# Performance work log

Hardware: AMD Instinct MI355X
Metric: run time of the kernel (lower is better)

The kernel has to match this reference:

```python
import jax, jax.numpy as jnp
import numpy as np

NBITS = 4
GROUP = 128
K = 4096   # in_features
N = 4096   # out_features
M = 4096   # flattened batch*seq tokens
EPS = 32 // NBITS  # elements per packed int32 = 8
MASK = (1 << NBITS) - 1  # unpack_mask = 15


def setup_inputs() -> dict:
    key = jax.random.key(0)
    k1, k2, k3, k4, k5 = jax.random.split(key, 5)
    x = jax.random.normal(k1, (M, K), dtype=jnp.float32)
    # raw 4-bit quantized weights, layout [K, N] (i.e. W_q.t() from the torch module)
    nib = jax.random.randint(k2, (K, N), 0, 1 << NBITS, dtype=jnp.int32)
    # pack EPS nibbles per int32 along K, matching pack(): element j gets shift j*NBITS
    nib = nib.reshape(K // EPS, EPS, N)
    shifts = (jnp.arange(EPS, dtype=jnp.int32) * NBITS)[None, :, None]
    parts = nib << shifts  # disjoint bit ranges
    W_q_packed = parts[:, 0]
    for j in range(1, EPS):
        W_q_packed = W_q_packed | parts[:, j]
    W_q_packed = W_q_packed.astype(jnp.int32)  # [K//EPS, N]
    # group-wise scales/zeros: [K//GROUP, N] (scales.view(N,-1).t() layout)
    scales = (jax.random.uniform(k3, (K // GROUP, N), dtype=jnp.float32) + 0.5) * 0.01
    zeros = jax.random.uniform(k4, (K // GROUP, N), dtype=jnp.float32) * MASK
    bias = jax.random.normal(k5, (N,), dtype=jnp.float32) * 0.1
    return {"x": x, "W_q_packed": W_q_packed, "scales": scales, "zeros": zeros, "bias": bias}


def reference(x, W_q_packed, scales, zeros, bias):
    # unpack: w[k, n] = (packed[k//EPS, n] >> ((k % EPS) * NBITS)) & MASK
    shifts = (jnp.arange(EPS, dtype=jnp.int32) * NBITS)[None, :, None]
    w = (W_q_packed[:, None, :] >> shifts) & MASK  # [K//EPS, EPS, N]
    w = w.reshape(K, N).astype(jnp.float32)
    # group-wise asymmetric dequant (W_group_mode == 3): W = (w - z) * s
    s = jnp.repeat(scales, GROUP, axis=0)  # [K, N]
    z = jnp.repeat(zeros, GROUP, axis=0)   # [K, N]
    W = (w - z) * s
    out = x @ W + bias  # [M, N]
    return out
```

## Files before the change

kernel.cpp:

```cpp
#include <hip/hip_runtime.h>
#include <stdint.h>


#define M_DIM 4096
#define N_DIM 4096
#define K_DIM 4096

typedef __attribute__((ext_vector_type(8))) short short8;
typedef __attribute__((ext_vector_type(4))) float f32x4;

__device__ __forceinline__ unsigned short f2bf(float f) {
  uint32_t u = __builtin_bit_cast(uint32_t, f);
  u += 0x7fffu + ((u >> 16) & 1u);
  return (unsigned short)(u >> 16);
}

__global__ __launch_bounds__(256) void prep_kernel(const float* __restrict__ x,
                                                   unsigned short* __restrict__ xb,
                                                   const int* __restrict__ Wq,
                                                   const float* __restrict__ scales,
                                                   const float* __restrict__ zeros,
                                                   unsigned short* __restrict__ wt) {
  __shared__ uint4 Ts[32 * 64];
  const int tid = threadIdx.x;
  if (blockIdx.x < 2048) {
    const int total = (M_DIM * K_DIM) / 8;
    const float4* x4 = (const float4*)x;
    uint4* o8 = (uint4*)xb;
#pragma unroll
    for (int p = 0; p < 4; ++p) {
      int i = (p * 2048 + blockIdx.x) * 256 + tid;
      if (i < total) {
        float4 a = x4[2 * i], b = x4[2 * i + 1];
        uint4 o;
        o.x = (uint32_t)f2bf(a.x) | ((uint32_t)f2bf(a.y) << 16);
        o.y = (uint32_t)f2bf(a.z) | ((uint32_t)f2bf(a.w) << 16);
        o.z = (uint32_t)f2bf(b.x) | ((uint32_t)f2bf(b.y) << 16);
        o.w = (uint32_t)f2bf(b.z) | ((uint32_t)f2bf(b.w) << 16);
        o8[i] = o;
      }
    }
    return;
  }
  const int blk = blockIdx.x - 2048;
  const int n0 = (blk & 127) * 32;
  const int gk0 = (blk >> 7) * 64;

#pragma unroll
  for (int p = 0; p < 8; ++p) {
    int e = p * 256 + tid;
    int n_l = e & 31;
    int gk_l = e >> 5;
    int gk = gk0 + gk_l;
    int n = n0 + n_l;
    int g = gk >> 4;
    uint32_t q = (uint32_t)Wq[gk * N_DIM + n];
    float s = scales[g * N_DIM + n];
    float z = zeros[g * N_DIM + n];
    unsigned short b[8];
#pragma unroll
    for (int j = 0; j < 8; ++j) {
      float f = ((float)((q >> (4 * j)) & 15u) - z) * s;
      b[j] = f2bf(f);
    }
    uint4 cell;
    cell.x = (uint32_t)b[0] | ((uint32_t)b[1] << 16);
    cell.y = (uint32_t)b[2] | ((uint32_t)b[3] << 16);
    cell.z = (uint32_t)b[4] | ((uint32_t)b[5] << 16);
    cell.w = (uint32_t)b[6] | ((uint32_t)b[7] << 16);
    Ts[n_l * 64 + (gk_l ^ (n_l & 7))] = cell;
  }
  __syncthreads();
  uint4* dst = (uint4*)wt;
#pragma unroll
  for (int p = 0; p < 8; ++p) {
    int n_l = p * 4 + (tid >> 6);
    int gk_l = tid & 63;
    uint4 cell = Ts[n_l * 64 + (gk_l ^ (n_l & 7))];
    dst[(size_t)(n0 + n_l) * (K_DIM / 8) + (gk0 + gk_l)] = cell;
  }
}

__global__ __launch_bounds__(256) void gemm_bt_kernel(const unsigned short* __restrict__ A,
                                                      const unsigned short* __restrict__ Bt,
                                                      const float* __restrict__ bias,
                                                      float* __restrict__ C) {
  __shared__ short8 As[1024];
  __shared__ short8 Bs[1024];
  const int tid = threadIdx.x;
  const int lane = tid & 63;
  const int w = tid >> 6;
  const int wm = w >> 1, wn = w & 1;

  const int b = blockIdx.x;
  const int xcd = b & 7;
  const int loc = b >> 3;
  const int nt = xcd * 4 + (loc & 3);
  const int mt = loc >> 2;
  const int m0 = mt * 128;
  const int n0 = nt * 128;

  const int c0 = w * 256 + lane;
  const int row0 = c0 >> 3;
  const int kc0 = (c0 & 7) ^ (row0 & 7);
  const unsigned short* Ablk = A + (size_t)m0 * K_DIM;
  const unsigned short* Bblk = Bt + (size_t)n0 * K_DIM;
  const int voff = row0 * K_DIM + kc0 * 8;

  f32x4 acc[4][4] = {};

  const int fr = lane & 15;
  const int fc = lane >> 4;
  const int a_row8 = (wm * 64 + fr) * 8;
  const int b_row8 = (wn * 64 + fr) * 8;
  const int kx0 = fc ^ (fr & 7);
  const int kx1 = (4 + fc) ^ (fr & 7);

  for (int kk = 0; kk < K_DIM / 64; ++kk) {
    const int k0 = kk * 64;
    __syncthreads();
#pragma unroll
    for (int j = 0; j < 4; ++j) {
      __builtin_amdgcn_global_load_lds(
          (const __attribute__((address_space(1))) void*)(Ablk + voff + j * 8 * K_DIM + k0),
          (__attribute__((address_space(3))) void*)&As[c0 + j * 64], 16, 0, 0);
      __builtin_amdgcn_global_load_lds(
          (const __attribute__((address_space(1))) void*)(Bblk + voff + j * 8 * K_DIM + k0),
          (__attribute__((address_space(3))) void*)&Bs[c0 + j * 64], 16, 0, 0);
    }
    __syncthreads();

    {
      short8 af[4], bv[4];
#pragma unroll
      for (int mi = 0; mi < 4; ++mi) af[mi] = As[a_row8 + mi * 128 + kx0];
#pragma unroll
      for (int ni = 0; ni < 4; ++ni) bv[ni] = Bs[b_row8 + ni * 128 + kx0];
#pragma unroll
      for (int mi = 0; mi < 4; ++mi)
#pragma unroll
        for (int ni = 0; ni < 4; ++ni)
          acc[mi][ni] = __builtin_amdgcn_mfma_f32_16x16x32_bf16(af[mi], bv[ni], acc[mi][ni], 0, 0, 0);
    }
    {
      short8 af[4], bv[4];
#pragma unroll
      for (int mi = 0; mi < 4; ++mi) af[mi] = As[a_row8 + mi * 128 + kx1];
#pragma unroll
      for (int ni = 0; ni < 4; ++ni) bv[ni] = Bs[b_row8 + ni * 128 + kx1];
#pragma unroll
      for (int mi = 0; mi < 4; ++mi)
#pragma unroll
        for (int ni = 0; ni < 4; ++ni)
          acc[mi][ni] = __builtin_amdgcn_mfma_f32_16x16x32_bf16(af[mi], bv[ni], acc[mi][ni], 0, 0, 0);
    }
  }

  const int rr = (lane >> 4) * 4;
#pragma unroll
  for (int ni = 0; ni < 4; ++ni) {
    const int gn = n0 + wn * 64 + ni * 16 + fr;
    const float bvv = bias[gn];
#pragma unroll
    for (int mi = 0; mi < 4; ++mi) {
      const int gm = m0 + wm * 64 + mi * 16 + rr;
#pragma unroll
      for (int r = 0; r < 4; ++r)
        C[(size_t)(gm + r) * N_DIM + gn] = acc[mi][ni][r] + bvv;
    }
  }
}

extern "C" void kernel_launch(void* const* d_in, const int* in_sizes, int n_in,
                              void* d_out, int out_size, void* d_ws, size_t ws_size,
                              hipStream_t stream) {
  const float* x = (const float*)d_in[0];
  const int* wq = (const int*)d_in[1];
  const float* sc = (const float*)d_in[2];
  const float* zr = (const float*)d_in[3];
  const float* bias = (const float*)d_in[4];
  float* out = (float*)d_out;

  unsigned short* xb = (unsigned short*)d_ws;
  unsigned short* wt = (unsigned short*)((char*)d_ws + (size_t)M_DIM * K_DIM * 2);

  prep_kernel<<<dim3(3072), dim3(256), 0, stream>>>(x, xb, wq, sc, zr, wt);
  gemm_bt_kernel<<<dim3(1024), dim3(256), 0, stream>>>(xb, wt, bias, out);
}
```

Before: 304.4 us.

## Use 256x256 tiles with double-buffered LDS and phased MFMA scheduling

```diff
diff --git a/kernel.cpp b/kernel.cpp
--- a/kernel.cpp
+++ b/kernel.cpp
@@ -81,79 +81,123 @@
   }
 }
 
-__global__ __launch_bounds__(256) void gemm_bt_kernel(const unsigned short* __restrict__ A,
-                                                      const unsigned short* __restrict__ Bt,
-                                                      const float* __restrict__ bias,
-                                                      float* __restrict__ C) {
-  __shared__ short8 As[1024];
-  __shared__ short8 Bs[1024];
+
+#define STAGE4(DST, SRC)                                                         \
+  {                                                                              \
+    _Pragma("unroll") for (int j = 0; j < 4; ++j)                                \
+        __builtin_amdgcn_global_load_lds(                                        \
+            (const __attribute__((address_space(1))) void*)((SRC) +              \
+                                                            (size_t)j * 64 * K_DIM), \
+            (__attribute__((address_space(3))) void*)((DST) + tid + j * 512),    \
+            16, 0, 0);                                                           \
+  }
+
+#define LOADA(QM)                                                                \
+  {                                                                              \
+    _Pragma("unroll") for (int mi = 0; mi < 4; ++mi) {                           \
+      af[mi][0] = ASb[a_base + ((QM) * 4 + mi) * 128 + kx0];                     \
+      af[mi][1] = ASb[a_base + ((QM) * 4 + mi) * 128 + kx1];                     \
+    }                                                                            \
+  }
+
+#define LOADB(QN)                                                                \
+  {                                                                              \
+    _Pragma("unroll") for (int ni = 0; ni < 2; ++ni) {                           \
+      bv[ni][0] = BSb[b_base + ((QN) * 2 + ni) * 128 + kx0];                     \
+      bv[ni][1] = BSb[b_base + ((QN) * 2 + ni) * 128 + kx1];                     \
+    }                                                                            \
+  }
+
+#define MFMA16(QM, QN)                                                           \
+  {                                                                              \
+    _Pragma("unroll") for (int mi = 0; mi < 4; ++mi)                             \
+        _Pragma("unroll") for (int ni = 0; ni < 2; ++ni) {                       \
+      acc[(QM) * 4 + mi][(QN) * 2 + ni] = __builtin_amdgcn_mfma_f32_16x16x32_bf16( \
+          af[mi][0], bv[ni][0], acc[(QM) * 4 + mi][(QN) * 2 + ni], 0, 0, 0);     \
+      acc[(QM) * 4 + mi][(QN) * 2 + ni] = __builtin_amdgcn_mfma_f32_16x16x32_bf16( \
+          af[mi][1], bv[ni][1], acc[(QM) * 4 + mi][(QN) * 2 + ni], 0, 0, 0);     \
+    }                                                                            \
+  }
+
+#define PHASE_MFMA(QM, QN)                                                       \
+  {                                                                              \
+    __builtin_amdgcn_s_barrier();                                                \
+    __builtin_amdgcn_s_setprio(1);                                               \
+    MFMA16(QM, QN);                                                              \
+    __builtin_amdgcn_s_setprio(0);                                               \
+    __builtin_amdgcn_s_barrier();                                                \
+  }
+
+__global__ __launch_bounds__(512, 2) void gemm_bt_kernel(
+    const unsigned short* __restrict__ A, const unsigned short* __restrict__ Bt,
+    const float* __restrict__ bias, float* __restrict__ C) {
+  __shared__ short8 As[2 * 2048];
+  __shared__ short8 Bs[2 * 2048];
+
   const int tid = threadIdx.x;
   const int lane = tid & 63;
   const int w = tid >> 6;
-  const int wm = w >> 1, wn = w & 1;
+  const int wm = w >> 2;
+  const int wn = w & 3;
 
   const int b = blockIdx.x;
   const int xcd = b & 7;
   const int loc = b >> 3;
-  const int nt = xcd * 4 + (loc & 3);
-  const int mt = loc >> 2;
-  const int m0 = mt * 128;
-  const int n0 = nt * 128;
-
-  const int c0 = w * 256 + lane;
-  const int row0 = c0 >> 3;
-  const int kc0 = (c0 & 7) ^ (row0 & 7);
-  const unsigned short* Ablk = A + (size_t)m0 * K_DIM;
-  const unsigned short* Bblk = Bt + (size_t)n0 * K_DIM;
-  const int voff = row0 * K_DIM + kc0 * 8;
-
-  f32x4 acc[4][4] = {};
+  const int nt = xcd * 2 + (loc & 1);
+  const int mt = loc >> 1;
+  const int m0 = mt * 256;
+  const int n0 = nt * 256;
+
+  const int srow = tid >> 3;
+  const int skc = (tid & 7) ^ (srow & 7);
+  const unsigned short* Ablk = A + (size_t)m0 * K_DIM + (size_t)srow * K_DIM + skc * 8;
+  const unsigned short* Bblk = Bt + (size_t)n0 * K_DIM + (size_t)srow * K_DIM + skc * 8;
 
   const int fr = lane & 15;
   const int fc = lane >> 4;
-  const int a_row8 = (wm * 64 + fr) * 8;
-  const int b_row8 = (wn * 64 + fr) * 8;
-  const int kx0 = fc ^ (fr & 7);
-  const int kx1 = (4 + fc) ^ (fr & 7);
-
-  for (int kk = 0; kk < K_DIM / 64; ++kk) {
-    const int k0 = kk * 64;
-    __syncthreads();
-#pragma unroll
-    for (int j = 0; j < 4; ++j) {
-      __builtin_amdgcn_global_load_lds(
-          (const __attribute__((address_space(1))) void*)(Ablk + voff + j * 8 * K_DIM + k0),
-          (__attribute__((address_space(3))) void*)&As[c0 + j * 64], 16, 0, 0);
-      __builtin_amdgcn_global_load_lds(
-          (const __attribute__((address_space(1))) void*)(Bblk + voff + j * 8 * K_DIM + k0),
-          (__attribute__((address_space(3))) void*)&Bs[c0 + j * 64], 16, 0, 0);
-    }
-    __syncthreads();
-
-    {
-      short8 af[4], bv[4];
-#pragma unroll
-      for (int mi = 0; mi < 4; ++mi) af[mi] = As[a_row8 + mi * 128 + kx0];
-#pragma unroll
-      for (int ni = 0; ni < 4; ++ni) bv[ni] = Bs[b_row8 + ni * 128 + kx0];
-#pragma unroll
-      for (int mi = 0; mi < 4; ++mi)
-#pragma unroll
-        for (int ni = 0; ni < 4; ++ni)
-          acc[mi][ni] = __builtin_amdgcn_mfma_f32_16x16x32_bf16(af[mi], bv[ni], acc[mi][ni], 0, 0, 0);
-    }
-    {
-      short8 af[4], bv[4];
-#pragma unroll
-      for (int mi = 0; mi < 4; ++mi) af[mi] = As[a_row8 + mi * 128 + kx1];
-#pragma unroll
-      for (int ni = 0; ni < 4; ++ni) bv[ni] = Bs[b_row8 + ni * 128 + kx1];
-#pragma unroll
-      for (int mi = 0; mi < 4; ++mi)
-#pragma unroll
-        for (int ni = 0; ni < 4; ++ni)
-          acc[mi][ni] = __builtin_amdgcn_mfma_f32_16x16x32_bf16(af[mi], bv[ni], acc[mi][ni], 0, 0, 0);
-    }
+  const int frx = fr & 7;
+  const int a_base = (wm * 128 + fr) * 8;
+  const int b_base = (wn * 64 + fr) * 8;
+  const int kx0 = fc ^ frx;
+  const int kx1 = (4 + fc) ^ frx;
+
+  f32x4 acc[8][4] = {};
+  short8 af[4][2];
+  short8 bv[2][2];
+
+  STAGE4(As, Ablk);
+  STAGE4(Bs, Bblk);
+  asm volatile("s_waitcnt vmcnt(0)" ::: "memory");
+  __builtin_amdgcn_s_barrier();
+
+  for (int kt = 0; kt < K_DIM / 64; ++kt) {
+    const int cur = kt & 1;
+    const short8* ASb = As + cur * 2048;
+    const short8* BSb = Bs + cur * 2048;
+    short8* Anx = As + (cur ^ 1) * 2048;
+    short8* Bnx = Bs + (cur ^ 1) * 2048;
+    const bool pf = (kt + 1 < K_DIM / 64);
+    const size_t knext = (size_t)(kt + 1) * 64;
+
+    LOADA(0);
+    LOADB(0);
+    if (pf) STAGE4(Anx, Ablk + knext);
+    PHASE_MFMA(0, 0);
+
+    LOADB(1);
+    if (pf) STAGE4(Bnx, Bblk + knext);
+    PHASE_MFMA(0, 1);
+
+    LOADA(1);
+    PHASE_MFMA(1, 1);
+
+    LOADB(0);
+    __builtin_amdgcn_s_barrier();
+    __builtin_amdgcn_s_setprio(1);
+    MFMA16(1, 0);
+    __builtin_amdgcn_s_setprio(0);
+    asm volatile("s_waitcnt vmcnt(0)" ::: "memory");
+    __builtin_amdgcn_s_barrier();
   }
 
   const int rr = (lane >> 4) * 4;
@@ -162,8 +206,8 @@
     const int gn = n0 + wn * 64 + ni * 16 + fr;
     const float bvv = bias[gn];
 #pragma unroll
-    for (int mi = 0; mi < 4; ++mi) {
-      const int gm = m0 + wm * 64 + mi * 16 + rr;
+    for (int mi = 0; mi < 8; ++mi) {
+      const int gm = m0 + wm * 128 + mi * 16 + rr;
 #pragma unroll
       for (int r = 0; r < 4; ++r)
         C[(size_t)(gm + r) * N_DIM + gn] = acc[mi][ni][r] + bvv;
@@ -185,5 +229,5 @@
   unsigned short* wt = (unsigned short*)((char*)d_ws + (size_t)M_DIM * K_DIM * 2);
 
   prep_kernel<<<dim3(3072), dim3(256), 0, stream>>>(x, xb, wq, sc, zr, wt);
-  gemm_bt_kernel<<<dim3(1024), dim3(256), 0, stream>>>(xb, wt, bias, out);
-}
+  gemm_bt_kernel<<<dim3(256), dim3(512), 0, stream>>>(xb, wt, bias, out);
+}
```

Result: faster. 266.8 us (-12.3%).

## Rewrite GEMM with 256x256 tiles, 4-stage LDS ring and interleaved MFMA/load schedule

Applied to the files above, without the earlier changes.

```diff
diff --git a/kernel.cpp b/kernel.cpp
--- a/kernel.cpp
+++ b/kernel.cpp
@@ -81,94 +81,154 @@
   }
 }
 
-__global__ __launch_bounds__(256) void gemm_bt_kernel(const unsigned short* __restrict__ A,
-                                                      const unsigned short* __restrict__ Bt,
-                                                      const float* __restrict__ bias,
-                                                      float* __restrict__ C) {
-  __shared__ short8 As[1024];
-  __shared__ short8 Bs[1024];
+
+#define ASBUF(T) (As + ((T) & 3) * 1024)
+#define BSBUF(T) (Bs + ((T) & 3) * 1024)
+#define ASRC(T) (Asrc + (size_t)(T) * 32)
+#define BSRC(T) (Bsrc + (size_t)(T) * 32)
+
+#define GLDS(DST, SRC)                                                          \
+  __builtin_amdgcn_global_load_lds(                                             \
+      (const __attribute__((address_space(1))) void*)(SRC),                     \
+      (__attribute__((address_space(3))) void*)(DST), 16, 0, 0)
+
+#define RD_AF(T, DST, RB)                                                       \
+  {                                                                             \
+    _Pragma("unroll") for (int mi = 0; mi < 4; ++mi)                            \
+        DST[mi] = ASBUF(T)[a_b + (RB) * 512 + mi * 64];                         \
+  }
+
+#define RD_BV(T, DST, CB)                                                       \
+  {                                                                             \
+    _Pragma("unroll") for (int ni = 0; ni < 2; ++ni)                            \
+        DST[ni] = BSBUF(T)[b_b + (CB) * 512 + ni * 64];                         \
+  }
+
+#define MFMAQ(AF, BV, RB, CB)                                                   \
+  {                                                                             \
+    __builtin_amdgcn_s_setprio(1);                                              \
+    _Pragma("unroll") for (int mi = 0; mi < 4; ++mi)                            \
+        _Pragma("unroll") for (int ni = 0; ni < 2; ++ni)                        \
+            acc[(RB) * 4 + mi][(CB) * 2 + ni] =                                 \
+                __builtin_amdgcn_mfma_f32_16x16x32_bf16(                        \
+                    AF[mi], BV[ni], acc[(RB) * 4 + mi][(CB) * 2 + ni], 0, 0, 0);\
+    __builtin_amdgcn_s_setprio(0);                                              \
+  }
+
+#define SB0 __builtin_amdgcn_sched_barrier(0)
+#define VM2 asm volatile("s_waitcnt vmcnt(2)" ::: "memory")
+#define VM0 asm volatile("s_waitcnt vmcnt(0)" ::: "memory")
+
+#define TILE32(T, BV0C, BV0N, STG, RDN, VMW)                                    \
+  {                                                                             \
+                        \
+    RD_AF((T), afQ, 1);                                                         \
+    if (STG) GLDS(ASBUF((T) + 2) + tid, ASRC((T) + 2));                         \
+    SB0;                                                                        \
+    MFMAQ(afP, BV0C, 0, 0);                                                     \
+    SB0;                                                                        \
+                          \
+    if (STG) GLDS(ASBUF((T) + 2) + tid + 512, ASRC((T) + 2) + (size_t)128 * K_DIM); \
+    SB0;                                                                        \
+    MFMAQ(afP, bvQ, 0, 1);                                                      \
+    SB0;                                                                        \
+    VMW;                                                                        \
+    SB0;                                                                        \
+    __builtin_amdgcn_s_barrier();                                               \
+    SB0;                                                                        \
+                     \
+    if (RDN) RD_BV((T) + 1, BV0N, 0);                                           \
+    if (STG) GLDS(BSBUF((T) + 2) + tid, BSRC((T) + 2));                         \
+    SB0;                                                                        \
+    MFMAQ(afQ, bvQ, 1, 1);                                                      \
+    SB0;                                                                        \
+             \
+    if (RDN) { RD_AF((T) + 1, afP, 0); RD_BV((T) + 1, bvQ, 1); }                \
+    if (STG) GLDS(BSBUF((T) + 2) + tid + 512, BSRC((T) + 2) + (size_t)128 * K_DIM); \
+    SB0;                                                                        \
+    MFMAQ(afQ, BV0C, 1, 0);                                                     \
+    SB0;                                                                        \
+    __builtin_amdgcn_s_barrier();                      \
+    SB0;                                                                        \
+  }
+
+__global__ __launch_bounds__(512, 2) void gemm_bt_kernel(
+    const unsigned short* __restrict__ A, const unsigned short* __restrict__ Bt,
+    const float* __restrict__ bias, float* __restrict__ C) {
+  __shared__ short8 As[4 * 1024];
+  __shared__ short8 Bs[4 * 1024];
+
   const int tid = threadIdx.x;
   const int lane = tid & 63;
   const int w = tid >> 6;
-  const int wm = w >> 1, wn = w & 1;
+  const int wm = w >> 2;
+  const int wn = w & 3;
 
   const int b = blockIdx.x;
   const int xcd = b & 7;
   const int loc = b >> 3;
-  const int nt = xcd * 4 + (loc & 3);
-  const int mt = loc >> 2;
-  const int m0 = mt * 128;
-  const int n0 = nt * 128;
-
-  const int c0 = w * 256 + lane;
-  const int row0 = c0 >> 3;
-  const int kc0 = (c0 & 7) ^ (row0 & 7);
-  const unsigned short* Ablk = A + (size_t)m0 * K_DIM;
-  const unsigned short* Bblk = Bt + (size_t)n0 * K_DIM;
-  const int voff = row0 * K_DIM + kc0 * 8;
-
-  f32x4 acc[4][4] = {};
+  const int nt = xcd * 2 + (loc & 1);
+  const int mt = loc >> 1;
+  const int m0 = mt * 256;
+  const int n0 = nt * 256;
+
+  const int srow = tid >> 2;
+  const int skc = (tid & 3) ^ ((srow >> 1) & 3);
+  const unsigned short* Asrc = A + (size_t)(m0 + srow) * K_DIM + skc * 8;
+  const unsigned short* Bsrc = Bt + (size_t)(n0 + srow) * K_DIM + skc * 8;
 
   const int fr = lane & 15;
   const int fc = lane >> 4;
-  const int a_row8 = (wm * 64 + fr) * 8;
-  const int b_row8 = (wn * 64 + fr) * 8;
-  const int kx0 = fc ^ (fr & 7);
-  const int kx1 = (4 + fc) ^ (fr & 7);
-
-  for (int kk = 0; kk < K_DIM / 64; ++kk) {
-    const int k0 = kk * 64;
-    __syncthreads();
-#pragma unroll
-    for (int j = 0; j < 4; ++j) {
-      __builtin_amdgcn_global_load_lds(
-          (const __attribute__((address_space(1))) void*)(Ablk + voff + j * 8 * K_DIM + k0),
-          (__attribute__((address_space(3))) void*)&As[c0 + j * 64], 16, 0, 0);
-      __builtin_amdgcn_global_load_lds(
-          (const __attribute__((address_space(1))) void*)(Bblk + voff + j * 8 * K_DIM + k0),
-          (__attribute__((address_space(3))) void*)&Bs[c0 + j * 64], 16, 0, 0);
+  const int kxs = fc ^ ((fr >> 1) & 3);
+  const int a_b = (wm * 64 + fr) * 4 + kxs;
+  const int b_b = (wn * 32 + fr) * 4 + kxs;
+
+  f32x4 acc[8][4] = {};
+  short8 afP[4], afQ[4];
+  short8 bv0a[2], bv0b[2];
+  short8 bvQ[2];
+
+  GLDS(ASBUF(0) + tid, ASRC(0));
+  GLDS(ASBUF(0) + tid + 512, ASRC(0) + (size_t)128 * K_DIM);
+  GLDS(BSBUF(0) + tid, BSRC(0));
+  GLDS(BSBUF(0) + tid + 512, BSRC(0) + (size_t)128 * K_DIM);
+  GLDS(ASBUF(1) + tid, ASRC(1));
+  GLDS(ASBUF(1) + tid + 512, ASRC(1) + (size_t)128 * K_DIM);
+  GLDS(BSBUF(1) + tid, BSRC(1));
+  GLDS(BSBUF(1) + tid + 512, BSRC(1) + (size_t)128 * K_DIM);
+  asm volatile("s_waitcnt vmcnt(4)" ::: "memory");
+  SB0;
+  __builtin_amdgcn_s_barrier();
+  SB0;
+  RD_BV(0, bv0a, 0);
+  RD_AF(0, afP, 0);
+  RD_BV(0, bvQ, 1);
+  SB0;
+
+  for (int t = 0; t < 126; t += 2) {
+    TILE32(t, bv0a, bv0b, 1, 1, VM2);
+    TILE32(t + 1, bv0b, bv0a, 1, 1, VM2);
+  }
+  TILE32(126, bv0a, bv0b, 0, 1, VM0);
+  TILE32(127, bv0b, bv0a, 0, 0, (void)0);
+
+  const int rr = (lane >> 4) * 4;
+#pragma unroll
+  for (int cb = 0; cb < 2; ++cb)
+#pragma unroll
+    for (int ni = 0; ni < 2; ++ni) {
+      const int gn = n0 + cb * 128 + wn * 32 + ni * 16 + fr;
+      const float bvv = bias[gn];
+#pragma unroll
+      for (int rb = 0; rb < 2; ++rb)
+#pragma unroll
+        for (int mi = 0; mi < 4; ++mi) {
+          const int gm = m0 + rb * 128 + wm * 64 + mi * 16 + rr;
+#pragma unroll
+          for (int r = 0; r < 4; ++r)
+            C[(size_t)(gm + r) * N_DIM + gn] = acc[rb * 4 + mi][cb * 2 + ni][r] + bvv;
+        }
     }
-    __syncthreads();
-
-    {
-      short8 af[4], bv[4];
-#pragma unroll
-      for (int mi = 0; mi < 4; ++mi) af[mi] = As[a_row8 + mi * 128 + kx0];
-#pragma unroll
-      for (int ni = 0; ni < 4; ++ni) bv[ni] = Bs[b_row8 + ni * 128 + kx0];
-#pragma unroll
-      for (int mi = 0; mi < 4; ++mi)
-#pragma unroll
-        for (int ni = 0; ni < 4; ++ni)
-          acc[mi][ni] = __builtin_amdgcn_mfma_f32_16x16x32_bf16(af[mi], bv[ni], acc[mi][ni], 0, 0, 0);
-    }
-    {
-      short8 af[4], bv[4];
-#pragma unroll
-      for (int mi = 0; mi < 4; ++mi) af[mi] = As[a_row8 + mi * 128 + kx1];
-#pragma unroll
-      for (int ni = 0; ni < 4; ++ni) bv[ni] = Bs[b_row8 + ni * 128 + kx1];
-#pragma unroll
-      for (int mi = 0; mi < 4; ++mi)
-#pragma unroll
-        for (int ni = 0; ni < 4; ++ni)
-          acc[mi][ni] = __builtin_amdgcn_mfma_f32_16x16x32_bf16(af[mi], bv[ni], acc[mi][ni], 0, 0, 0);
-    }
-  }
-
-  const int rr = (lane >> 4) * 4;
-#pragma unroll
-  for (int ni = 0; ni < 4; ++ni) {
-    const int gn = n0 + wn * 64 + ni * 16 + fr;
-    const float bvv = bias[gn];
-#pragma unroll
-    for (int mi = 0; mi < 4; ++mi) {
-      const int gm = m0 + wm * 64 + mi * 16 + rr;
-#pragma unroll
-      for (int r = 0; r < 4; ++r)
-        C[(size_t)(gm + r) * N_DIM + gn] = acc[mi][ni][r] + bvv;
-    }
-  }
 }
 
 extern "C" void kernel_launch(void* const* d_in, const int* in_sizes, int n_in,
@@ -185,5 +245,5 @@
   unsigned short* wt = (unsigned short*)((char*)d_ws + (size_t)M_DIM * K_DIM * 2);
 
   prep_kernel<<<dim3(3072), dim3(256), 0, stream>>>(x, xb, wq, sc, zr, wt);
-  gemm_bt_kernel<<<dim3(1024), dim3(256), 0, stream>>>(xb, wt, bias, out);
-}
+  gemm_bt_kernel<<<dim3(256), dim3(512), 0, stream>>>(xb, wt, bias, out);
+}
```

Measured after the change: 259.1 us. 1.17x faster.

## Double-buffer GEMM LDS with 256x128 tiles, 512 threads, split prep kernels

Applied to the files above, without the earlier changes.

```diff
diff --git a/kernel.cpp b/kernel.cpp
--- a/kernel.cpp
+++ b/kernel.cpp
@@ -15,34 +15,34 @@
   return (unsigned short)(u >> 16);
 }
 
-__global__ __launch_bounds__(256) void prep_kernel(const float* __restrict__ x,
-                                                   unsigned short* __restrict__ xb,
-                                                   const int* __restrict__ Wq,
-                                                   const float* __restrict__ scales,
-                                                   const float* __restrict__ zeros,
-                                                   unsigned short* __restrict__ wt) {
+__global__ __launch_bounds__(256) void cvt_kernel(const float* __restrict__ x,
+                                                  unsigned short* __restrict__ xb) {
+  const int tid = threadIdx.x;
+  const int total = (M_DIM * K_DIM) / 8;
+  const float4* x4 = (const float4*)x;
+  uint4* o8 = (uint4*)xb;
+#pragma unroll
+  for (int p = 0; p < 4; ++p) {
+    int i = (p * 2048 + blockIdx.x) * 256 + tid;
+    if (i < total) {
+      float4 a = x4[2 * i], b = x4[2 * i + 1];
+      uint4 o;
+      o.x = (uint32_t)f2bf(a.x) | ((uint32_t)f2bf(a.y) << 16);
+      o.y = (uint32_t)f2bf(a.z) | ((uint32_t)f2bf(a.w) << 16);
+      o.z = (uint32_t)f2bf(b.x) | ((uint32_t)f2bf(b.y) << 16);
+      o.w = (uint32_t)f2bf(b.z) | ((uint32_t)f2bf(b.w) << 16);
+      o8[i] = o;
+    }
+  }
+}
+
+__global__ __launch_bounds__(256) void dequant_kernel(const int* __restrict__ Wq,
+                                                      const float* __restrict__ scales,
+                                                      const float* __restrict__ zeros,
+                                                      unsigned short* __restrict__ wt) {
   __shared__ uint4 Ts[32 * 64];
   const int tid = threadIdx.x;
-  if (blockIdx.x < 2048) {
-    const int total = (M_DIM * K_DIM) / 8;
-    const float4* x4 = (const float4*)x;
-    uint4* o8 = (uint4*)xb;
-#pragma unroll
-    for (int p = 0; p < 4; ++p) {
-      int i = (p * 2048 + blockIdx.x) * 256 + tid;
-      if (i < total) {
-        float4 a = x4[2 * i], b = x4[2 * i + 1];
-        uint4 o;
-        o.x = (uint32_t)f2bf(a.x) | ((uint32_t)f2bf(a.y) << 16);
-        o.y = (uint32_t)f2bf(a.z) | ((uint32_t)f2bf(a.w) << 16);
-        o.z = (uint32_t)f2bf(b.x) | ((uint32_t)f2bf(b.y) << 16);
-        o.w = (uint32_t)f2bf(b.z) | ((uint32_t)f2bf(b.w) << 16);
-        o8[i] = o;
-      }
-    }
-    return;
-  }
-  const int blk = blockIdx.x - 2048;
+  const int blk = blockIdx.x;
   const int n0 = (blk & 127) * 32;
   const int gk0 = (blk >> 7) * 64;
 
@@ -81,78 +81,89 @@
   }
 }
 
-__global__ __launch_bounds__(256) void gemm_bt_kernel(const unsigned short* __restrict__ A,
-                                                      const unsigned short* __restrict__ Bt,
-                                                      const float* __restrict__ bias,
-                                                      float* __restrict__ C) {
-  __shared__ short8 As[1024];
-  __shared__ short8 Bs[1024];
+
+#define ASBUF(T) (As + ((T) & 1) * 1024)
+#define BSBUF(T) (Bs + ((T) & 1) * 512)
+
+#define GLDS(DST, SRC)                                                          \
+  __builtin_amdgcn_global_load_lds(                                             \
+      (const __attribute__((address_space(1))) void*)(SRC),                     \
+      (__attribute__((address_space(3))) void*)(DST), 16, 0, 0)
+
+#define STAGE(T)                                                                \
+  {                                                                             \
+    const unsigned short* as = Asrc + (size_t)(T) * 32;                         \
+    const unsigned short* bs = Bsrc + (size_t)(T) * 32;                         \
+    GLDS(ASBUF(T) + tid, as);                                                   \
+    GLDS(ASBUF(T) + tid + 512, as + (size_t)128 * K_DIM);                       \
+    GLDS(BSBUF(T) + tid, bs);                                                   \
+  }
+
+#define SB0 __builtin_amdgcn_sched_barrier(0)
+
+__global__ __launch_bounds__(512, 4) void gemm_bt_kernel(
+    const unsigned short* __restrict__ A, const unsigned short* __restrict__ Bt,
+    const float* __restrict__ bias, float* __restrict__ C) {
+  __shared__ short8 As[2 * 1024];
+  __shared__ short8 Bs[2 * 512];
+
   const int tid = threadIdx.x;
   const int lane = tid & 63;
   const int w = tid >> 6;
-  const int wm = w >> 1, wn = w & 1;
+  const int wm = w >> 1;
+  const int wn = w & 1;
 
   const int b = blockIdx.x;
   const int xcd = b & 7;
   const int loc = b >> 3;
   const int nt = xcd * 4 + (loc & 3);
   const int mt = loc >> 2;
-  const int m0 = mt * 128;
+  const int m0 = mt * 256;
   const int n0 = nt * 128;
 
-  const int c0 = w * 256 + lane;
-  const int row0 = c0 >> 3;
-  const int kc0 = (c0 & 7) ^ (row0 & 7);
-  const unsigned short* Ablk = A + (size_t)m0 * K_DIM;
-  const unsigned short* Bblk = Bt + (size_t)n0 * K_DIM;
-  const int voff = row0 * K_DIM + kc0 * 8;
-
-  f32x4 acc[4][4] = {};
+  const int srow = tid >> 2;
+  const int skc = (tid & 3) ^ ((srow >> 1) & 3);
+  const unsigned short* Asrc = A + (size_t)(m0 + srow) * K_DIM + skc * 8;
+  const unsigned short* Bsrc = Bt + (size_t)(n0 + srow) * K_DIM + skc * 8;
 
   const int fr = lane & 15;
   const int fc = lane >> 4;
-  const int a_row8 = (wm * 64 + fr) * 8;
-  const int b_row8 = (wn * 64 + fr) * 8;
-  const int kx0 = fc ^ (fr & 7);
-  const int kx1 = (4 + fc) ^ (fr & 7);
-
-  for (int kk = 0; kk < K_DIM / 64; ++kk) {
-    const int k0 = kk * 64;
-    __syncthreads();
-#pragma unroll
-    for (int j = 0; j < 4; ++j) {
-      __builtin_amdgcn_global_load_lds(
-          (const __attribute__((address_space(1))) void*)(Ablk + voff + j * 8 * K_DIM + k0),
-          (__attribute__((address_space(3))) void*)&As[c0 + j * 64], 16, 0, 0);
-      __builtin_amdgcn_global_load_lds(
-          (const __attribute__((address_space(1))) void*)(Bblk + voff + j * 8 * K_DIM + k0),
-          (__attribute__((address_space(3))) void*)&Bs[c0 + j * 64], 16, 0, 0);
-    }
-    __syncthreads();
-
-    {
-      short8 af[4], bv[4];
-#pragma unroll
-      for (int mi = 0; mi < 4; ++mi) af[mi] = As[a_row8 + mi * 128 + kx0];
-#pragma unroll
-      for (int ni = 0; ni < 4; ++ni) bv[ni] = Bs[b_row8 + ni * 128 + kx0];
-#pragma unroll
-      for (int mi = 0; mi < 4; ++mi)
-#pragma unroll
-        for (int ni = 0; ni < 4; ++ni)
-          acc[mi][ni] = __builtin_amdgcn_mfma_f32_16x16x32_bf16(af[mi], bv[ni], acc[mi][ni], 0, 0, 0);
-    }
-    {
-      short8 af[4], bv[4];
-#pragma unroll
-      for (int mi = 0; mi < 4; ++mi) af[mi] = As[a_row8 + mi * 128 + kx1];
-#pragma unroll
-      for (int ni = 0; ni < 4; ++ni) bv[ni] = Bs[b_row8 + ni * 128 + kx1];
-#pragma unroll
-      for (int mi = 0; mi < 4; ++mi)
-#pragma unroll
-        for (int ni = 0; ni < 4; ++ni)
-          acc[mi][ni] = __builtin_amdgcn_mfma_f32_16x16x32_bf16(af[mi], bv[ni], acc[mi][ni], 0, 0, 0);
+  const int kxs = fc ^ ((fr >> 1) & 3);
+  const int a_b = (wm * 64 + fr) * 4 + kxs;
+  const int b_b = (wn * 64 + fr) * 4 + kxs;
+
+  f32x4 acc[4][4] = {};
+
+  STAGE(0);
+  asm volatile("s_waitcnt vmcnt(0)" ::: "memory");
+  SB0;
+  __builtin_amdgcn_s_barrier();
+
+  for (int t = 0; t < 128; ++t) {
+    if (t < 127) STAGE(t + 1);
+
+    const short8* ASb = ASBUF(t);
+    const short8* BSb = BSBUF(t);
+    short8 af[4], bv[4];
+#pragma unroll
+    for (int mi = 0; mi < 4; ++mi) af[mi] = ASb[a_b + mi * 64];
+#pragma unroll
+    for (int ni = 0; ni < 4; ++ni) bv[ni] = BSb[b_b + ni * 64];
+
+    __builtin_amdgcn_s_setprio(1);
+#pragma unroll
+    for (int mi = 0; mi < 4; ++mi)
+#pragma unroll
+      for (int ni = 0; ni < 4; ++ni)
+        acc[mi][ni] = __builtin_amdgcn_mfma_f32_16x16x32_bf16(af[mi], bv[ni],
+                                                              acc[mi][ni], 0, 0, 0);
+    __builtin_amdgcn_s_setprio(0);
+
+    if (t < 127) {
+      asm volatile("s_waitcnt vmcnt(0)" ::: "memory");
+      SB0;
+      __builtin_amdgcn_s_barrier();
+      SB0;
     }
   }
 
@@ -184,6 +195,7 @@
   unsigned short* xb = (unsigned short*)d_ws;
   unsigned short* wt = (unsigned short*)((char*)d_ws + (size_t)M_DIM * K_DIM * 2);
 
-  prep_kernel<<<dim3(3072), dim3(256), 0, stream>>>(x, xb, wq, sc, zr, wt);
-  gemm_bt_kernel<<<dim3(1024), dim3(256), 0, stream>>>(xb, wt, bias, out);
-}
+  cvt_kernel<<<dim3(2048), dim3(256), 0, stream>>>(x, xb);
+  dequant_kernel<<<dim3(1024), dim3(256), 0, stream>>>(wq, sc, zr, wt);
+  gemm_bt_kernel<<<dim3(512), dim3(512), 0, stream>>>(xb, wt, bias, out);
+}
```

Measured after the change: 269.4 us. -11.5%, faster.
